# Kernel optimization log

Measured on AMD Instinct MI355X. Metric: run time of the kernel, lower is better.

The kernel has to match this reference:

```python
import jax, jax.numpy as jnp
import numpy as np

EPS = 1e-7


def ciou_pairwise(b1, b2):
    # b1: (N,1,4), b2: (1,N,4) in xyxy; returns (N,N) CIoU
    b1x1, b1y1, b1x2, b1y2 = b1[..., 0], b1[..., 1], b1[..., 2], b1[..., 3]
    b2x1, b2y1, b2x2, b2y2 = b2[..., 0], b2[..., 1], b2[..., 2], b2[..., 3]

    # intersection
    iw = jnp.clip(jnp.minimum(b1x2, b2x2) - jnp.maximum(b1x1, b2x1), 0.0)
    ih = jnp.clip(jnp.minimum(b1y2, b2y2) - jnp.maximum(b1y1, b2y1), 0.0)
    inter = iw * ih

    w1, h1 = b1x2 - b1x1, b1y2 - b1y1
    w2, h2 = b2x2 - b2x1, b2y2 - b2y1
    union = w1 * h1 + w2 * h2 - inter + EPS
    iou = inter / union

    # smallest enclosing box diagonal
    cw = jnp.maximum(b1x2, b2x2) - jnp.minimum(b1x1, b2x1)
    ch = jnp.maximum(b1y2, b2y2) - jnp.minimum(b1y1, b2y1)
    c2 = cw * cw + ch * ch + EPS

    # squared center distance
    rho2 = ((b2x1 + b2x2 - b1x1 - b1x2) ** 2 + (b2y1 + b2y2 - b1y1 - b1y2) ** 2) / 4.0

    # aspect-ratio consistency term
    v = (4.0 / (np.pi ** 2)) * (jnp.arctan(w2 / (h2 + EPS)) - jnp.arctan(w1 / (h1 + EPS))) ** 2
    alpha = jax.lax.stop_gradient(v / (v - iou + (1.0 + EPS)))
    return iou - (rho2 / c2 + v * alpha)


def setup_inputs() -> dict:
    key = jax.random.key(0)
    k1, k2, k3 = jax.random.split(key, 3)
    N = 4096
    conf = jax.random.uniform(k1, (N, 1), dtype=jnp.float32)           # confidence in [0,1)
    xy1 = jax.random.uniform(k2, (N, 2), dtype=jnp.float32) * 600.0    # top-left corner
    wh = jax.random.uniform(k3, (N, 2), dtype=jnp.float32) * 100.0 + 1.0  # width/height >= 1
    x = jnp.concatenate([conf, xy1, xy1 + wh], axis=1)                 # (N, 5): conf, x1, y1, x2, y2
    gamma = jnp.zeros((1,), dtype=jnp.float32)
    return {"x": x, "gamma": gamma}


def reference(x, gamma):
    boxes = x[:, 1:]
    conf = x[:, 0]
    iou = ciou_pairwise(boxes[:, None, :], boxes[None, :, :])          # (N, N)
    conf_matrix = conf[:, None] * conf[None, :]                        # (N, N) outer product
    attention = jax.nn.softmax(iou * conf_matrix, axis=-1)             # (N, N)
    x_prime = x * gamma + attention @ x                                # (N, 5)
    return jax.nn.sigmoid(x_prime)
```

## Files before the change

kernel.cpp:

```cpp
#include <hip/hip_runtime.h>
#include <math.h>

#define N 4096
#define FEPS 1e-7f
#define ROWS 8
#define BLK 256
#define FSTRIDE 12

__global__ void precompute_kernel(const float* __restrict__ x, float* __restrict__ f) {
    int i = blockIdx.x * blockDim.x + threadIdx.x;
    if (i >= N) return;
    float cf = x[i * 5 + 0], x1 = x[i * 5 + 1], y1 = x[i * 5 + 2];
    float x2 = x[i * 5 + 3], y2 = x[i * 5 + 4];
    float w = x2 - x1, h = y2 - y1;
    float* fi = f + (size_t)i * FSTRIDE;
    fi[0] = cf; fi[1] = x1; fi[2] = y1; fi[3] = x2; fi[4] = y2;
    fi[5] = x1 + x2; fi[6] = y1 + y2; fi[7] = w; fi[8] = h;
    fi[9] = w * h + FEPS;
    fi[10] = atanf(w / (h + FEPS));
    fi[11] = w * h;
}

__global__ __launch_bounds__(BLK) void ciou_attn_kernel(
        const float* __restrict__ x,
        const float* __restrict__ f,
        const float* __restrict__ gamma,
        float* __restrict__ out) {
    const int tid = threadIdx.x;
    const int i0 = blockIdx.x * ROWS;

    float rx1[ROWS], ry1[ROWS], rx2[ROWS], ry2[ROWS], rsx[ROWS], rsy[ROWS];
    float rw[ROWS], rh[ROWS], rar[ROWS], rat[ROWS], rcf[ROWS];
#pragma unroll
    for (int r = 0; r < ROWS; r++) {
        const float* fi = f + (size_t)(i0 + r) * FSTRIDE;
        rcf[r] = fi[0]; rx1[r] = fi[1]; ry1[r] = fi[2]; rx2[r] = fi[3]; ry2[r] = fi[4];
        rsx[r] = fi[5]; rsy[r] = fi[6]; rw[r] = fi[7]; rh[r] = fi[8];
        rar[r] = fi[11]; rat[r] = fi[10];
    }

    float sum[ROWS];
    float acc[ROWS][5];
#pragma unroll
    for (int r = 0; r < ROWS; r++) {
        sum[r] = 0.f;
#pragma unroll
        for (int c = 0; c < 5; c++) acc[r][c] = 0.f;
    }

    const float K = 0.4052847345693511f;
    const float ONEP = 1.f + FEPS;

#pragma unroll 2
    for (int j = tid; j < N; j += BLK) {
        const float4* fj = (const float4*)(f + (size_t)j * FSTRIDE);
        float4 A = fj[0], B = fj[1], C = fj[2];
        float jcf = A.x, jx1 = A.y, jy1 = A.z, jx2 = A.w;
        float jy2 = B.x, jsx = B.y, jsy = B.z, jw = B.w;
        float jh = C.x, jar2 = C.y, jat = C.z;
#pragma unroll
        for (int r = 0; r < ROWS; r++) {
            float iwr = fminf(rx2[r], jx2) - fmaxf(rx1[r], jx1);
            float ihr = fminf(ry2[r], jy2) - fmaxf(ry1[r], jy1);
            float iw = fmaxf(iwr, 0.f);
            float ih = fmaxf(ihr, 0.f);
            float inter = iw * ih;
            float uni = (rar[r] + jar2) - inter;
            float iou = fminf(inter * __builtin_amdgcn_rcpf(uni), 1.0f);
            float cw = (rw[r] + jw) - iwr;
            float ch = (rh[r] + jh) - ihr;
            float c2 = cw * cw + ch * ch + FEPS;
            float dx = jsx - rsx[r];
            float dy = jsy - rsy[r];
            float rho2 = (dx * dx + dy * dy) * 0.25f;
            float da = jat - rat[r];
            float v = K * da * da;
            float den = (v - iou) + ONEP;
            float valpha = v * v * __builtin_amdgcn_rcpf(den);
            float ciou = iou - (rho2 * __builtin_amdgcn_rcpf(c2) + valpha);
            float e = __expf(ciou * rcf[r] * jcf);
            sum[r] += e;
            acc[r][0] += e * jcf;
            acc[r][1] += e * jx1;
            acc[r][2] += e * jy1;
            acc[r][3] += e * jx2;
            acc[r][4] += e * jy2;
        }
    }

    __shared__ float red[BLK / 64][ROWS * 6];
    const int wave = tid >> 6;
    const int lane = tid & 63;
#pragma unroll
    for (int r = 0; r < ROWS; r++) {
        float v6[6] = {sum[r], acc[r][0], acc[r][1], acc[r][2], acc[r][3], acc[r][4]};
#pragma unroll
        for (int k = 0; k < 6; k++) {
            float val = v6[k];
#pragma unroll
            for (int off = 32; off > 0; off >>= 1) val += __shfl_down(val, off, 64);
            if (lane == 0) red[wave][r * 6 + k] = val;
        }
    }
    __syncthreads();
    if (tid < ROWS * 6) {
        float tot = 0.f;
#pragma unroll
        for (int w = 0; w < BLK / 64; w++) tot += red[w][tid];
        red[0][tid] = tot;
    }
    __syncthreads();
    if (tid < ROWS * 5) {
        int r = tid / 5, c = tid % 5;
        int i = i0 + r;
        float se = red[0][r * 6];
        float a = red[0][r * 6 + 1 + c];
        float xp = x[(size_t)i * 5 + c] * gamma[0] + a / se;
        out[(size_t)i * 5 + c] = 1.f / (1.f + expf(-xp));
    }
}

extern "C" void kernel_launch(void* const* d_in, const int* in_sizes, int n_in,
                              void* d_out, int out_size, void* d_ws, size_t ws_size,
                              hipStream_t stream) {
    const float* x = (const float*)d_in[0];
    const float* gamma = (const float*)d_in[1];
    float* out = (float*)d_out;
    float* f = (float*)d_ws;

    precompute_kernel<<<(N + 255) / 256, 256, 0, stream>>>(x, f);
    ciou_attn_kernel<<<N / ROWS, BLK, 0, stream>>>(x, f, gamma, out);
}
```

Measured before the change: 92.27 us.

## Split column range across blocks and merge the partials in an epilogue kernel

```diff
diff --git a/kernel.cpp b/kernel.cpp
--- a/kernel.cpp
+++ b/kernel.cpp
@@ -5,7 +5,10 @@
 #define FEPS 1e-7f
 #define ROWS 8
 #define BLK 256
+#define JT 2
 #define FSTRIDE 12
+
+#define PART_OFF (N * FSTRIDE)
 
 __global__ void precompute_kernel(const float* __restrict__ x, float* __restrict__ f) {
     int i = blockIdx.x * blockDim.x + threadIdx.x;
@@ -22,12 +25,12 @@
 }
 
 __global__ __launch_bounds__(BLK) void ciou_attn_kernel(
-        const float* __restrict__ x,
         const float* __restrict__ f,
-        const float* __restrict__ gamma,
-        float* __restrict__ out) {
+        float* __restrict__ part) {
     const int tid = threadIdx.x;
-    const int i0 = blockIdx.x * ROWS;
+    const int g = blockIdx.x / JT;
+    const int jt = blockIdx.x % JT;
+    const int i0 = g * ROWS;
 
     float rx1[ROWS], ry1[ROWS], rx2[ROWS], ry2[ROWS], rsx[ROWS], rsy[ROWS];
     float rw[ROWS], rh[ROWS], rar[ROWS], rat[ROWS], rcf[ROWS];
@@ -50,9 +53,10 @@
 
     const float K = 0.4052847345693511f;
     const float ONEP = 1.f + FEPS;
+    const int jend = (jt + 1) * (N / JT);
 
 #pragma unroll 2
-    for (int j = tid; j < N; j += BLK) {
+    for (int j = jt * (N / JT) + tid; j < jend; j += BLK) {
         const float4* fj = (const float4*)(f + (size_t)j * FSTRIDE);
         float4 A = fj[0], B = fj[1], C = fj[2];
         float jcf = A.x, jx1 = A.y, jy1 = A.z, jx2 = A.w;
@@ -76,8 +80,8 @@
             float da = jat - rat[r];
             float v = K * da * da;
             float den = (v - iou) + ONEP;
-            float valpha = v * v * __builtin_amdgcn_rcpf(den);
-            float ciou = iou - (rho2 * __builtin_amdgcn_rcpf(c2) + valpha);
+            float numer = rho2 * den + (v * v) * c2;
+            float ciou = iou - numer * __builtin_amdgcn_rcpf(c2 * den);
             float e = __expf(ciou * rcf[r] * jcf);
             sum[r] += e;
             acc[r][0] += e * jcf;
@@ -107,17 +111,27 @@
         float tot = 0.f;
 #pragma unroll
         for (int w = 0; w < BLK / 64; w++) tot += red[w][tid];
-        red[0][tid] = tot;
+        part[(size_t)blockIdx.x * (ROWS * 6) + tid] = tot;
     }
-    __syncthreads();
-    if (tid < ROWS * 5) {
-        int r = tid / 5, c = tid % 5;
-        int i = i0 + r;
-        float se = red[0][r * 6];
-        float a = red[0][r * 6 + 1 + c];
-        float xp = x[(size_t)i * 5 + c] * gamma[0] + a / se;
-        out[(size_t)i * 5 + c] = 1.f / (1.f + expf(-xp));
+}
+
+__global__ void epilogue_kernel(const float* __restrict__ x,
+                                const float* __restrict__ gamma,
+                                const float* __restrict__ part,
+                                float* __restrict__ out) {
+    int idx = blockIdx.x * blockDim.x + threadIdx.x;
+    if (idx >= N * 5) return;
+    int i = idx / 5, c = idx % 5;
+    int g = i >> 3, r = i & 7;
+    float se = 0.f, a = 0.f;
+#pragma unroll
+    for (int jt = 0; jt < JT; jt++) {
+        const float* p = part + (size_t)(g * JT + jt) * (ROWS * 6) + r * 6;
+        se += p[0];
+        a += p[1 + c];
     }
+    float xp = x[idx] * gamma[0] + a / se;
+    out[idx] = 1.f / (1.f + expf(-xp));
 }
 
 extern "C" void kernel_launch(void* const* d_in, const int* in_sizes, int n_in,
@@ -127,7 +141,9 @@
     const float* gamma = (const float*)d_in[1];
     float* out = (float*)d_out;
     float* f = (float*)d_ws;
+    float* part = (float*)d_ws + PART_OFF;
 
     precompute_kernel<<<(N + 255) / 256, 256, 0, stream>>>(x, f);
-    ciou_attn_kernel<<<N / ROWS, BLK, 0, stream>>>(x, f, gamma, out);
+    ciou_attn_kernel<<<(N / ROWS) * JT, BLK, 0, stream>>>(f, part);
+    epilogue_kernel<<<(N * 5 + 255) / 256, 256, 0, stream>>>(x, gamma, part, out);
 }
```

Result: slower. 125.0 us (+35.4%).
